# Kernel tuning notes

Measured on AMD Instinct MI355X. Metric: run time of the kernel, lower is better.

Reference implementation:

```python
import jax, jax.numpy as jnp
import numpy as np

B, S, N = 1, 128, 256
C_IN, C_H, C_OUT = 256, 32, 128
EPS = 1e-5


def setup_inputs() -> dict:
    key = jax.random.key(0)
    k_m, k_wa, k_wb, k_wo = jax.random.split(key, 4)
    m = jax.random.normal(k_m, (B, S, N, C_IN), dtype=jnp.float32)
    mask = jnp.ones((B, S, N), dtype=jnp.float32)
    gamma = jnp.ones((C_IN,), dtype=jnp.float32)
    beta = jnp.zeros((C_IN,), dtype=jnp.float32)
    # nn.Linear weights are (out, in)
    Wa = jax.random.normal(k_wa, (C_H, C_IN), dtype=jnp.float32) / np.sqrt(C_IN).astype(np.float32)
    Wb = jax.random.normal(k_wb, (C_H, C_IN), dtype=jnp.float32) / np.sqrt(C_IN).astype(np.float32)
    # proj_o is final_init (zeros) in the source; use small random weights so the
    # baseline output is non-trivial for correctness checking.
    Wo = jax.random.normal(k_wo, (C_OUT, C_H * C_H), dtype=jnp.float32) / np.sqrt(C_H * C_H).astype(np.float32)
    bo = jnp.zeros((C_OUT,), dtype=jnp.float32)
    return {"m": m, "mask": mask, "gamma": gamma, "beta": beta,
            "Wa": Wa, "Wb": Wb, "Wo": Wo, "bo": bo}


def reference(m, mask, gamma, beta, Wa, Wb, Wo, bo):
    # LayerNorm over c_in
    mu = jnp.mean(m, axis=-1, keepdims=True)
    var = jnp.mean((m - mu) ** 2, axis=-1, keepdims=True)
    mn = (m - mu) * jax.lax.rsqrt(var + EPS) * gamma + beta  # (B,S,N,c_in)

    mk = mask[..., None]  # (B,S,N,1)
    a = jnp.einsum('bsni,hi->bsnh', mn, Wa) * mk  # (B,S,N,c_h)
    b = jnp.einsum('bsni,hi->bsnh', mn, Wb) * mk  # (B,S,N,c_h)

    # pairwise mask count over S, clamped to >= 1
    num_mask = jnp.clip(jnp.einsum('bsi,bsj->bij', mask, mask), 1.0, None)  # (B,N,N)

    # outer-product mean over the sequence dim
    z = jnp.einsum('bsic,bsjd->bijcd', a, b)  # (B,N,N,c_h,c_h)
    z = z.reshape(z.shape[0], z.shape[1], z.shape[2], C_H * C_H)
    z = z / num_mask[..., None]

    return jnp.einsum('bijk,ok->bijo', z, Wo) + bo  # (B,N,N,c_out)
```

## Files before the change

### kernel.cpp

```cpp
#include <hip/hip_runtime.h>
#include <hip/hip_bf16.h>

#define S_DIM 128
#define N_DIM 256
#define CIN   256
#define CH    32
#define COUT  128

typedef __attribute__((ext_vector_type(8))) short bf16x8;
typedef __attribute__((ext_vector_type(4))) float f32x4;
typedef __attribute__((ext_vector_type(16))) float f32x16;

__device__ __forceinline__ unsigned short f2bf(float f) {
  union { float f; unsigned int u; } v; v.f = f;
  unsigned int u = v.u;
  return (unsigned short)((u + 0x7FFFu + ((u >> 16) & 1u)) >> 16);
}

__device__ __forceinline__ unsigned int pk2(float x, float y) {
  float2 f2; f2.x = x; f2.y = y;
  __hip_bfloat162 h = __float22bfloat162_rn(f2);
  union { __hip_bfloat162 h; unsigned int u; } c; c.h = h;
  return c.u;
}

__global__ __launch_bounds__(256) void lnp_prep_kernel(
    const float* __restrict__ m, const float* __restrict__ mask,
    const float* __restrict__ gamma, const float* __restrict__ beta,
    const float* __restrict__ Wa, const float* __restrict__ Wb,
    const float* __restrict__ Wo,
    float* __restrict__ rnm, unsigned short* __restrict__ wo3,
    unsigned short* __restrict__ a_t, unsigned short* __restrict__ b_t) {
  const int b = blockIdx.x, t = threadIdx.x;
  if (b < 1024) {
    __shared__ __align__(16) unsigned short mn[32][264];
    __shared__ __align__(16) unsigned short wabs[64 * 256];
    const int i = b & 255, s0 = (b >> 8) * 32;
    const int w = t >> 6, l = t & 63, lq = l >> 4, lr = l & 15;

    #pragma unroll
    for (int it = 0; it < 8; it++) {
      const int gi = it * 256 + t;
      const int r = gi >> 5, g = gi & 31;
      const float* src = (r < 32) ? (Wa + r * 256 + g * 8)
                                  : (Wb + (r - 32) * 256 + g * 8);
      const int gp = (g & 16) | ((g ^ (r & 15)) & 15);
      unsigned short* dst = &wabs[r * 256 + gp * 8];
      const float4 v0 = *(const float4*)(src);
      const float4 v1 = *(const float4*)(src + 4);
      dst[0] = f2bf(v0.x); dst[1] = f2bf(v0.y); dst[2] = f2bf(v0.z); dst[3] = f2bf(v0.w);
      dst[4] = f2bf(v1.x); dst[5] = f2bf(v1.y); dst[6] = f2bf(v1.z); dst[7] = f2bf(v1.w);
    }

    const float4 g4 = *(const float4*)(gamma + l * 4);
    const float4 b4 = *(const float4*)(beta + l * 4);

    for (int rr = 0; rr < 8; rr++) {
      const int r = w * 8 + rr;
      const int s = s0 + r;
      const float4 v = *(const float4*)(m + ((size_t)(s * N_DIM + i)) * CIN + l * 4);
      float sum = v.x + v.y + v.z + v.w;
      float sq  = v.x * v.x + v.y * v.y + v.z * v.z + v.w * v.w;
      #pragma unroll
      for (int off = 32; off > 0; off >>= 1) {
        sum += __shfl_down(sum, off);
        sq  += __shfl_down(sq, off);
      }
      sum = __shfl(sum, 0); sq = __shfl(sq, 0);
      const float mu = sum * (1.0f / CIN);
      const float var = fmaxf(sq * (1.0f / CIN) - mu * mu, 0.0f);
      const float rs = rsqrtf(var + 1e-5f);
      const float mk = mask[s * N_DIM + i];
      ushort4 p;
      p.x = f2bf(((v.x - mu) * rs * g4.x + b4.x) * mk);
      p.y = f2bf(((v.y - mu) * rs * g4.y + b4.y) * mk);
      p.z = f2bf(((v.z - mu) * rs * g4.z + b4.z) * mk);
      p.w = f2bf(((v.w - mu) * rs * g4.w + b4.w) * mk);
      *(ushort4*)(&mn[r][l * 4]) = p;
    }
    __syncthreads();

    const int wm = w & 1;
    const int n2 = w >> 1;
    f32x4 acc0 = {0.f, 0.f, 0.f, 0.f}, acc1 = {0.f, 0.f, 0.f, 0.f};
    #pragma unroll
    for (int ks = 0; ks < 8; ks++) {
      const int k0 = ks * 32 + lq * 8;
      const int g = ks * 4 + lq;
      const int gp = (g & 16) | ((g ^ lr) & 15);
      const bf16x8 af = *(const bf16x8*)(&mn[wm * 16 + lr][k0]);
      const bf16x8 bf0 = *(const bf16x8*)(&wabs[(n2 * 32 + lr) * 256 + gp * 8]);
      const bf16x8 bf1 = *(const bf16x8*)(&wabs[(n2 * 32 + 16 + lr) * 256 + gp * 8]);
      acc0 = __builtin_amdgcn_mfma_f32_16x16x32_bf16(af, bf0, acc0, 0, 0, 0);
      acc1 = __builtin_amdgcn_mfma_f32_16x16x32_bf16(af, bf1, acc1, 0, 0, 0);
    }

    unsigned short* dst = (n2 == 0) ? a_t : b_t;
    const int scol = s0 + wm * 16 + lq * 4;
    ushort4 q0, q1;
    q0.x = f2bf(acc0[0]); q0.y = f2bf(acc0[1]); q0.z = f2bf(acc0[2]); q0.w = f2bf(acc0[3]);
    q1.x = f2bf(acc1[0]); q1.y = f2bf(acc1[1]); q1.z = f2bf(acc1[2]); q1.w = f2bf(acc1[3]);
    *(ushort4*)(dst + ((size_t)(i * CH + lr)) * S_DIM + scol) = q0;
    *(ushort4*)(dst + ((size_t)(i * CH + 16 + lr)) * S_DIM + scol) = q1;
  } else if (b < 1152) {
    const int r = b - 1024;
    #pragma unroll
    for (int q = 0; q < 4; q++) {
      const int f = r * 1024 + q * 256 + t;
      const int e = f & 7, l = (f >> 3) & 63;
      const int step = (f >> 9) & 63, og = f >> 15;
      const int kp = step * 16 + (l >> 5) * 8 + e;
      const int c = kp & 31, d = kp >> 5;
      const int o = og * 32 + (l & 31);
      wo3[f] = f2bf(Wo[o * 1024 + c * 32 + d]);
    }
  } else {
    const int i = b - 1152;
    float acc = 0.f;
    #pragma unroll 8
    for (int s = 0; s < S_DIM; s++)
      acc += mask[s * N_DIM + i] * mask[s * N_DIM + t];
    acc = fmaxf(acc, 1.0f);
    rnm[i * N_DIM + t] = 1.0f / acc;
  }
}

__global__ __launch_bounds__(512, 4) void fused_kernel(
    const unsigned short* __restrict__ a_t, const unsigned short* __restrict__ b_t,
    const unsigned short* __restrict__ wo3, const float* __restrict__ rnm,
    const float* __restrict__ bo, float* __restrict__ out) {
  extern __shared__ __align__(16) unsigned short smem[];
  unsigned short* sA = smem;
  unsigned short* sB = smem + 16384;
  unsigned short* sZ = smem;
  float* fpart = (float*)smem;

  const int t = threadIdx.x, w = t >> 6, l = t & 63;
  const int lq = l >> 4, lr = l & 15;
  const int bx = blockIdx.x, by = blockIdx.y;

  const unsigned short* srcA = a_t + (size_t)bx * 32768;
  const unsigned short* srcB = b_t + (size_t)by * 16384;

  const int og = w & 3, kh = w >> 2;
  const int pA = l & 31;
  const unsigned short* wop =
      wo3 + ((size_t)(og * 64 + kh * 32) * 64 + l) * 8;

  const int wy = (w >> 1) * 64, wx = (w & 1) * 64;
  f32x4 acc[4][4];
  #pragma unroll
  for (int a = 0; a < 4; a++)
    #pragma unroll
    for (int c = 0; c < 4; c++) acc[a][c] = (f32x4){0.f, 0.f, 0.f, 0.f};

  #pragma unroll 1
  for (int h = 0; h < 2; h++) {
    if (h) __syncthreads();
    #pragma unroll
    for (int it = 0; it < 4; it++) {
      const int idx = it * 512 + t;
      const int r = idx >> 3, g = idx & 7;
      const bf16x8 v = *(const bf16x8*)(srcA + r * 128 + h * 64 + g * 8);
      *(bf16x8*)(&sA[r * 64 + ((g ^ (r & 7)) << 3)]) = v;
    }
    #pragma unroll
    for (int it = 0; it < 2; it++) {
      const int idx = it * 512 + t;
      const int r = idx >> 3, g = idx & 7;
      const bf16x8 v = *(const bf16x8*)(srcB + r * 128 + h * 64 + g * 8);
      *(bf16x8*)(&sB[r * 64 + ((g ^ (r & 7)) << 3)]) = v;
    }
    __syncthreads();

    #pragma unroll
    for (int ks2 = 0; ks2 < 2; ks2++) {
      const int gi = ks2 * 4 + lq;
      bf16x8 afr[4], bfr[4];
      #pragma unroll
      for (int a = 0; a < 4; a++) {
        const int ra = wy + a * 16 + lr;
        afr[a] = *(const bf16x8*)(&sA[ra * 64 + ((gi ^ (ra & 7)) << 3)]);
        const int rb = wx + a * 16 + lr;
        bfr[a] = *(const bf16x8*)(&sB[rb * 64 + ((gi ^ (rb & 7)) << 3)]);
      }
      #pragma unroll
      for (int a = 0; a < 4; a++)
        #pragma unroll
        for (int c = 0; c < 4; c++)
          acc[a][c] = __builtin_amdgcn_mfma_f32_16x16x32_bf16(afr[a], bfr[c], acc[a][c], 0, 0, 0);
    }
  }

  bf16x8 wfb0[4], wfb1[4];
  #pragma unroll
  for (int q = 0; q < 4; q++)
    wfb0[q] = *(const bf16x8*)(wop + (size_t)q * 512);

  __syncthreads();

  #pragma unroll
  for (int a = 0; a < 4; a++) {
    #pragma unroll
    for (int c = 0; c < 4; c++) {
      const int zrb = wy + a * 16 + lq * 4;
      const int zc  = wx + c * 16 + lr;
      const int pr = (zrb >> 5) * 4 + (zc >> 5);
      const int off = (zc & 31) * 32 + (zrb & 31);
      const int g = off >> 3;
      const int gp = (g & ~7) | ((g ^ (g >> 3) ^ pr) & 7);
      uint2 q;
      q.x = pk2(acc[a][c][0], acc[a][c][1]);
      q.y = pk2(acc[a][c][2], acc[a][c][3]);
      *(uint2*)(&sZ[pr * 1024 + gp * 8 + (off & 7)]) = q;
    }
  }
  __syncthreads();

  #pragma unroll
  for (int q = 0; q < 4; q++)
    wfb1[q] = *(const bf16x8*)(wop + (size_t)(4 + q) * 512);

  const int pair = t >> 4;
  const int ob   = (t & 15) * 8;
  const int ii = bx * 8 + (pair >> 2), jj = by * 4 + (pair & 3);
  const float sc = rnm[ii * N_DIM + jj];
  const float4 bo0 = *(const float4*)(bo + ob);
  const float4 bo1 = *(const float4*)(bo + ob + 4);

  f32x16 acc2;
  #pragma unroll
  for (int r = 0; r < 16; r++) acc2[r] = 0.f;

  #pragma unroll
  for (int jb = 0; jb < 8; jb++) {
    #pragma unroll
    for (int q = 0; q < 4; q++) {
      const int j = jb * 4 + q;
      const int s = kh * 32 + j;
      const int g = s * 2 + (l >> 5);
      const int gA = (g & ~7) | ((g ^ (g >> 3) ^ pA) & 7);
      const bf16x8 zf = *(const bf16x8*)(&sZ[pA * 1024 + gA * 8]);
      const bf16x8 wf = (jb & 1) ? wfb1[q] : wfb0[q];
      acc2 = __builtin_amdgcn_mfma_f32_32x32x16_bf16(zf, wf, acc2, 0, 0, 0);
    }
    if (jb < 6) {
      #pragma unroll
      for (int q = 0; q < 4; q++) {
        const bf16x8 v = *(const bf16x8*)(wop + (size_t)((jb + 2) * 4 + q) * 512);
        if (jb & 1) wfb1[q] = v; else wfb0[q] = v;
      }
    }
  }
  __syncthreads();

  const int oc = og * 32 + (l & 31);
  #pragma unroll
  for (int r = 0; r < 16; r++) {
    const int row = (r & 3) + 8 * (r >> 2) + 4 * (l >> 5);
    fpart[kh * 4224 + row * 132 + oc] = acc2[r];
  }
  __syncthreads();

  const int fb = pair * 132 + ob;
  f32x4 u0 = {0.f, 0.f, 0.f, 0.f}, u1 = {0.f, 0.f, 0.f, 0.f};
  #pragma unroll
  for (int q = 0; q < 2; q++) {
    u0 += *(const f32x4*)(&fpart[q * 4224 + fb]);
    u1 += *(const f32x4*)(&fpart[q * 4224 + fb + 4]);
  }
  float* po = out + ((size_t)(ii * N_DIM + jj)) * COUT + ob;
  float4 w0, w1;
  w0.x = u0[0] * sc + bo0.x; w0.y = u0[1] * sc + bo0.y;
  w0.z = u0[2] * sc + bo0.z; w0.w = u0[3] * sc + bo0.w;
  w1.x = u1[0] * sc + bo1.x; w1.y = u1[1] * sc + bo1.y;
  w1.z = u1[2] * sc + bo1.z; w1.w = u1[3] * sc + bo1.w;
  *(float4*)(po)     = w0;
  *(float4*)(po + 4) = w1;
}

extern "C" void kernel_launch(void* const* d_in, const int* in_sizes, int n_in,
                              void* d_out, int out_size, void* d_ws, size_t ws_size,
                              hipStream_t stream) {
  const float* m     = (const float*)d_in[0];
  const float* mask  = (const float*)d_in[1];
  const float* gamma = (const float*)d_in[2];
  const float* beta  = (const float*)d_in[3];
  const float* Wa    = (const float*)d_in[4];
  const float* Wb    = (const float*)d_in[5];
  const float* Wo    = (const float*)d_in[6];
  const float* bo    = (const float*)d_in[7];
  float* out = (float*)d_out;

  char* ws = (char*)d_ws;
  float*          rnm = (float*)(ws);
  unsigned short* wo3 = (unsigned short*)(ws + 262144);
  unsigned short* a_t = (unsigned short*)(ws + 524288);
  unsigned short* b_t = (unsigned short*)(ws + 2621440);

  hipFuncSetAttribute((const void*)fused_kernel,
                      hipFuncAttributeMaxDynamicSharedMemorySize, 65536);

  lnp_prep_kernel<<<1408, 256, 0, stream>>>(m, mask, gamma, beta, Wa, Wb, Wo,
                                            rnm, wo3, a_t, b_t);
  fused_kernel<<<dim3(32, 64), 512, 65536, stream>>>(a_t, b_t, wo3, rnm, bo, out);
}
```

Measured before the change: 144.6 us.

## Double-buffer S-chunk loads in fused kernel and pack bf16 conversions in prep

The fused outer-product kernel now splits the S=128 reduction into four 32-wide chunks held in two ping-pong LDS buffers. The global loads for the next chunk are issued into registers before the MFMA work on the current chunk, so load latency overlaps compute instead of stalling between halves. The prep kernel now converts to bf16 with paired conversions written as vector stores, and issues all eight row loads of m and mask before the LayerNorm math. The cost is one more barrier per chunk, more live registers, and more complex LDS indexing.

```diff
diff --git a/kernel.cpp b/kernel.cpp
--- a/kernel.cpp
+++ b/kernel.cpp
@@ -45,20 +45,30 @@
       const float* src = (r < 32) ? (Wa + r * 256 + g * 8)
                                   : (Wb + (r - 32) * 256 + g * 8);
       const int gp = (g & 16) | ((g ^ (r & 15)) & 15);
-      unsigned short* dst = &wabs[r * 256 + gp * 8];
       const float4 v0 = *(const float4*)(src);
       const float4 v1 = *(const float4*)(src + 4);
-      dst[0] = f2bf(v0.x); dst[1] = f2bf(v0.y); dst[2] = f2bf(v0.z); dst[3] = f2bf(v0.w);
-      dst[4] = f2bf(v1.x); dst[5] = f2bf(v1.y); dst[6] = f2bf(v1.z); dst[7] = f2bf(v1.w);
+      uint4 qv;
+      qv.x = pk2(v0.x, v0.y); qv.y = pk2(v0.z, v0.w);
+      qv.z = pk2(v1.x, v1.y); qv.w = pk2(v1.z, v1.w);
+      *(uint4*)(&wabs[r * 256 + gp * 8]) = qv;
     }
 
     const float4 g4 = *(const float4*)(gamma + l * 4);
     const float4 b4 = *(const float4*)(beta + l * 4);
 
+    float4 mv[8];
+    float mkv[8];
+    #pragma unroll
+    for (int rr = 0; rr < 8; rr++) {
+      const int s = s0 + w * 8 + rr;
+      mv[rr] = *(const float4*)(m + ((size_t)(s * N_DIM + i)) * CIN + l * 4);
+      mkv[rr] = mask[s * N_DIM + i];
+    }
+
+    #pragma unroll
     for (int rr = 0; rr < 8; rr++) {
       const int r = w * 8 + rr;
-      const int s = s0 + r;
-      const float4 v = *(const float4*)(m + ((size_t)(s * N_DIM + i)) * CIN + l * 4);
+      const float4 v = mv[rr];
       float sum = v.x + v.y + v.z + v.w;
       float sq  = v.x * v.x + v.y * v.y + v.z * v.z + v.w * v.w;
       #pragma unroll
@@ -70,13 +80,13 @@
       const float mu = sum * (1.0f / CIN);
       const float var = fmaxf(sq * (1.0f / CIN) - mu * mu, 0.0f);
       const float rs = rsqrtf(var + 1e-5f);
-      const float mk = mask[s * N_DIM + i];
-      ushort4 p;
-      p.x = f2bf(((v.x - mu) * rs * g4.x + b4.x) * mk);
-      p.y = f2bf(((v.y - mu) * rs * g4.y + b4.y) * mk);
-      p.z = f2bf(((v.z - mu) * rs * g4.z + b4.z) * mk);
-      p.w = f2bf(((v.w - mu) * rs * g4.w + b4.w) * mk);
-      *(ushort4*)(&mn[r][l * 4]) = p;
+      const float mk = mkv[rr];
+      uint2 p2;
+      p2.x = pk2(((v.x - mu) * rs * g4.x + b4.x) * mk,
+                 ((v.y - mu) * rs * g4.y + b4.y) * mk);
+      p2.y = pk2(((v.z - mu) * rs * g4.z + b4.z) * mk,
+                 ((v.w - mu) * rs * g4.w + b4.w) * mk);
+      *(uint2*)(&mn[r][l * 4]) = p2;
     }
     __syncthreads();
 
@@ -97,11 +107,11 @@
 
     unsigned short* dst = (n2 == 0) ? a_t : b_t;
     const int scol = s0 + wm * 16 + lq * 4;
-    ushort4 q0, q1;
-    q0.x = f2bf(acc0[0]); q0.y = f2bf(acc0[1]); q0.z = f2bf(acc0[2]); q0.w = f2bf(acc0[3]);
-    q1.x = f2bf(acc1[0]); q1.y = f2bf(acc1[1]); q1.z = f2bf(acc1[2]); q1.w = f2bf(acc1[3]);
-    *(ushort4*)(dst + ((size_t)(i * CH + lr)) * S_DIM + scol) = q0;
-    *(ushort4*)(dst + ((size_t)(i * CH + 16 + lr)) * S_DIM + scol) = q1;
+    uint2 q0, q1;
+    q0.x = pk2(acc0[0], acc0[1]); q0.y = pk2(acc0[2], acc0[3]);
+    q1.x = pk2(acc1[0], acc1[1]); q1.y = pk2(acc1[2], acc1[3]);
+    *(uint2*)(dst + ((size_t)(i * CH + lr)) * S_DIM + scol) = q0;
+    *(uint2*)(dst + ((size_t)(i * CH + 16 + lr)) * S_DIM + scol) = q1;
   } else if (b < 1152) {
     const int r = b - 1024;
     #pragma unroll
@@ -130,8 +140,10 @@
     const unsigned short* __restrict__ wo3, const float* __restrict__ rnm,
     const float* __restrict__ bo, float* __restrict__ out) {
   extern __shared__ __align__(16) unsigned short smem[];
-  unsigned short* sA = smem;
-  unsigned short* sB = smem + 16384;
+  unsigned short* sA0 = smem;
+  unsigned short* sA1 = smem + 8192;
+  unsigned short* sB0 = smem + 16384;
+  unsigned short* sB1 = smem + 20480;
   unsigned short* sZ = smem;
   float* fpart = (float*)smem;
 
@@ -154,50 +166,62 @@
     #pragma unroll
     for (int c = 0; c < 4; c++) acc[a][c] = (f32x4){0.f, 0.f, 0.f, 0.f};
 
-  #pragma unroll 1
-  for (int h = 0; h < 2; h++) {
-    if (h) __syncthreads();
-    #pragma unroll
-    for (int it = 0; it < 4; it++) {
-      const int idx = it * 512 + t;
-      const int r = idx >> 3, g = idx & 7;
-      const bf16x8 v = *(const bf16x8*)(srcA + r * 128 + h * 64 + g * 8);
-      *(bf16x8*)(&sA[r * 64 + ((g ^ (r & 7)) << 3)]) = v;
-    }
-    #pragma unroll
-    for (int it = 0; it < 2; it++) {
-      const int idx = it * 512 + t;
-      const int r = idx >> 3, g = idx & 7;
-      const bf16x8 v = *(const bf16x8*)(srcB + r * 128 + h * 64 + g * 8);
-      *(bf16x8*)(&sB[r * 64 + ((g ^ (r & 7)) << 3)]) = v;
-    }
-    __syncthreads();
-
-    #pragma unroll
-    for (int ks2 = 0; ks2 < 2; ks2++) {
-      const int gi = ks2 * 4 + lq;
-      bf16x8 afr[4], bfr[4];
-      #pragma unroll
-      for (int a = 0; a < 4; a++) {
-        const int ra = wy + a * 16 + lr;
-        afr[a] = *(const bf16x8*)(&sA[ra * 64 + ((gi ^ (ra & 7)) << 3)]);
-        const int rb = wx + a * 16 + lr;
-        bfr[a] = *(const bf16x8*)(&sB[rb * 64 + ((gi ^ (rb & 7)) << 3)]);
-      }
-      #pragma unroll
-      for (int a = 0; a < 4; a++)
-        #pragma unroll
-        for (int c = 0; c < 4; c++)
-          acc[a][c] = __builtin_amdgcn_mfma_f32_16x16x32_bf16(afr[a], bfr[c], acc[a][c], 0, 0, 0);
-    }
-  }
+  bf16x8 ldA0, ldA1, ldB0;
+  const int sr = t >> 2, sg = t & 3;
+  const int swz = ((sg ^ sr) & 3) << 3;
+
+#define ISSUE_CH(c) do { \
+    ldA0 = *(const bf16x8*)(srcA + sr * 128 + (c) * 32 + sg * 8); \
+    ldA1 = *(const bf16x8*)(srcA + (128 + sr) * 128 + (c) * 32 + sg * 8); \
+    ldB0 = *(const bf16x8*)(srcB + sr * 128 + (c) * 32 + sg * 8); \
+  } while (0)
+
+#define WRITE_CH(c) do { \
+    unsigned short* dA = ((c) & 1) ? sA1 : sA0; \
+    unsigned short* dB = ((c) & 1) ? sB1 : sB0; \
+    *(bf16x8*)(&dA[sr * 32 + swz]) = ldA0; \
+    *(bf16x8*)(&dA[(128 + sr) * 32 + swz]) = ldA1; \
+    *(bf16x8*)(&dB[sr * 32 + swz]) = ldB0; \
+  } while (0)
+
+#define COMPUTE_CH(c) do { \
+    const unsigned short* pa = ((c) & 1) ? sA1 : sA0; \
+    const unsigned short* pb = ((c) & 1) ? sB1 : sB0; \
+    bf16x8 afr[4], bfr[4]; \
+    _Pragma("unroll") \
+    for (int a2 = 0; a2 < 4; a2++) { \
+      const int ra = wy + a2 * 16 + lr; \
+      afr[a2] = *(const bf16x8*)(&pa[ra * 32 + (((lq ^ ra) & 3) << 3)]); \
+      const int rb = wx + a2 * 16 + lr; \
+      bfr[a2] = *(const bf16x8*)(&pb[rb * 32 + (((lq ^ rb) & 3) << 3)]); \
+    } \
+    _Pragma("unroll") \
+    for (int a2 = 0; a2 < 4; a2++) \
+      _Pragma("unroll") \
+      for (int c2 = 0; c2 < 4; c2++) \
+        acc[a2][c2] = __builtin_amdgcn_mfma_f32_16x16x32_bf16(afr[a2], bfr[c2], acc[a2][c2], 0, 0, 0); \
+  } while (0)
+
+  ISSUE_CH(0);
+  WRITE_CH(0);
+  ISSUE_CH(1);
+  __syncthreads();
+
+  WRITE_CH(1); ISSUE_CH(2); COMPUTE_CH(0); __syncthreads();
+  WRITE_CH(2); ISSUE_CH(3); COMPUTE_CH(1); __syncthreads();
+  WRITE_CH(3);              COMPUTE_CH(2); __syncthreads();
 
   bf16x8 wfb0[4], wfb1[4];
   #pragma unroll
   for (int q = 0; q < 4; q++)
     wfb0[q] = *(const bf16x8*)(wop + (size_t)q * 512);
 
-  __syncthreads();
+  COMPUTE_CH(3);
+  __syncthreads();
+
+#undef ISSUE_CH
+#undef WRITE_CH
+#undef COMPUTE_CH
 
   #pragma unroll
   for (int a = 0; a < 4; a++) {
```

Result: slower. 154.8 us (+7.0%).

## Drop split-K reduction in output projection; vectorize bf16 packing and batch loads

Applied to the files above, without the earlier changes.

The second GEMM stage (z times Wo) now runs on only 4 waves, each covering the full K=1024 instead of half, which removes the LDS partial-sum buffer, two barriers and the cross-wave reduction. Each wave writes its outputs directly to global memory with per-element scale and bias, so stores become scalar and strided rather than float4. The prep kernel packs bf16 pairs with wide LDS/global stores and issues all LayerNorm row loads up front to raise memory-level parallelism. The trade-off is that half the waves sit idle in the second GEMM and the dependent MFMA chain doubles in length.

```diff
diff --git a/kernel.cpp b/kernel.cpp
--- a/kernel.cpp
+++ b/kernel.cpp
@@ -45,20 +45,30 @@
       const float* src = (r < 32) ? (Wa + r * 256 + g * 8)
                                   : (Wb + (r - 32) * 256 + g * 8);
       const int gp = (g & 16) | ((g ^ (r & 15)) & 15);
-      unsigned short* dst = &wabs[r * 256 + gp * 8];
       const float4 v0 = *(const float4*)(src);
       const float4 v1 = *(const float4*)(src + 4);
-      dst[0] = f2bf(v0.x); dst[1] = f2bf(v0.y); dst[2] = f2bf(v0.z); dst[3] = f2bf(v0.w);
-      dst[4] = f2bf(v1.x); dst[5] = f2bf(v1.y); dst[6] = f2bf(v1.z); dst[7] = f2bf(v1.w);
+      uint4 qv;
+      qv.x = pk2(v0.x, v0.y); qv.y = pk2(v0.z, v0.w);
+      qv.z = pk2(v1.x, v1.y); qv.w = pk2(v1.z, v1.w);
+      *(uint4*)(&wabs[r * 256 + gp * 8]) = qv;
     }
 
     const float4 g4 = *(const float4*)(gamma + l * 4);
     const float4 b4 = *(const float4*)(beta + l * 4);
 
+    float4 mv[8];
+    float mkv[8];
+    #pragma unroll
+    for (int rr = 0; rr < 8; rr++) {
+      const int s = s0 + w * 8 + rr;
+      mv[rr] = *(const float4*)(m + ((size_t)(s * N_DIM + i)) * CIN + l * 4);
+      mkv[rr] = mask[s * N_DIM + i];
+    }
+
+    #pragma unroll
     for (int rr = 0; rr < 8; rr++) {
       const int r = w * 8 + rr;
-      const int s = s0 + r;
-      const float4 v = *(const float4*)(m + ((size_t)(s * N_DIM + i)) * CIN + l * 4);
+      const float4 v = mv[rr];
       float sum = v.x + v.y + v.z + v.w;
       float sq  = v.x * v.x + v.y * v.y + v.z * v.z + v.w * v.w;
       #pragma unroll
@@ -70,13 +80,13 @@
       const float mu = sum * (1.0f / CIN);
       const float var = fmaxf(sq * (1.0f / CIN) - mu * mu, 0.0f);
       const float rs = rsqrtf(var + 1e-5f);
-      const float mk = mask[s * N_DIM + i];
-      ushort4 p;
-      p.x = f2bf(((v.x - mu) * rs * g4.x + b4.x) * mk);
-      p.y = f2bf(((v.y - mu) * rs * g4.y + b4.y) * mk);
-      p.z = f2bf(((v.z - mu) * rs * g4.z + b4.z) * mk);
-      p.w = f2bf(((v.w - mu) * rs * g4.w + b4.w) * mk);
-      *(ushort4*)(&mn[r][l * 4]) = p;
+      const float mk = mkv[rr];
+      uint2 p2;
+      p2.x = pk2(((v.x - mu) * rs * g4.x + b4.x) * mk,
+                 ((v.y - mu) * rs * g4.y + b4.y) * mk);
+      p2.y = pk2(((v.z - mu) * rs * g4.z + b4.z) * mk,
+                 ((v.w - mu) * rs * g4.w + b4.w) * mk);
+      *(uint2*)(&mn[r][l * 4]) = p2;
     }
     __syncthreads();
 
@@ -97,11 +107,11 @@
 
     unsigned short* dst = (n2 == 0) ? a_t : b_t;
     const int scol = s0 + wm * 16 + lq * 4;
-    ushort4 q0, q1;
-    q0.x = f2bf(acc0[0]); q0.y = f2bf(acc0[1]); q0.z = f2bf(acc0[2]); q0.w = f2bf(acc0[3]);
-    q1.x = f2bf(acc1[0]); q1.y = f2bf(acc1[1]); q1.z = f2bf(acc1[2]); q1.w = f2bf(acc1[3]);
-    *(ushort4*)(dst + ((size_t)(i * CH + lr)) * S_DIM + scol) = q0;
-    *(ushort4*)(dst + ((size_t)(i * CH + 16 + lr)) * S_DIM + scol) = q1;
+    uint2 q0, q1;
+    q0.x = pk2(acc0[0], acc0[1]); q0.y = pk2(acc0[2], acc0[3]);
+    q1.x = pk2(acc1[0], acc1[1]); q1.y = pk2(acc1[2], acc1[3]);
+    *(uint2*)(dst + ((size_t)(i * CH + lr)) * S_DIM + scol) = q0;
+    *(uint2*)(dst + ((size_t)(i * CH + 16 + lr)) * S_DIM + scol) = q1;
   } else if (b < 1152) {
     const int r = b - 1024;
     #pragma unroll
@@ -133,7 +143,6 @@
   unsigned short* sA = smem;
   unsigned short* sB = smem + 16384;
   unsigned short* sZ = smem;
-  float* fpart = (float*)smem;
 
   const int t = threadIdx.x, w = t >> 6, l = t & 63;
   const int lq = l >> 4, lr = l & 15;
@@ -142,10 +151,9 @@
   const unsigned short* srcA = a_t + (size_t)bx * 32768;
   const unsigned short* srcB = b_t + (size_t)by * 16384;
 
-  const int og = w & 3, kh = w >> 2;
+  const int og = w & 3;
   const int pA = l & 31;
-  const unsigned short* wop =
-      wo3 + ((size_t)(og * 64 + kh * 32) * 64 + l) * 8;
+  const unsigned short* wop = wo3 + ((size_t)(og * 64) * 64 + l) * 8;
 
   const int wy = (w >> 1) * 64, wx = (w & 1) * 64;
   f32x4 acc[4][4];
@@ -193,9 +201,11 @@
   }
 
   bf16x8 wfb0[4], wfb1[4];
-  #pragma unroll
-  for (int q = 0; q < 4; q++)
-    wfb0[q] = *(const bf16x8*)(wop + (size_t)q * 512);
+  if (w < 4) {
+    #pragma unroll
+    for (int q = 0; q < 4; q++)
+      wfb0[q] = *(const bf16x8*)(wop + (size_t)q * 512);
+  }
 
   __syncthreads();
 
@@ -217,34 +227,38 @@
   }
   __syncthreads();
 
+  if (w >= 4) return;
+
   #pragma unroll
   for (int q = 0; q < 4; q++)
     wfb1[q] = *(const bf16x8*)(wop + (size_t)(4 + q) * 512);
 
-  const int pair = t >> 4;
-  const int ob   = (t & 15) * 8;
-  const int ii = bx * 8 + (pair >> 2), jj = by * 4 + (pair & 3);
-  const float sc = rnm[ii * N_DIM + jj];
-  const float4 bo0 = *(const float4*)(bo + ob);
-  const float4 bo1 = *(const float4*)(bo + ob + 4);
+  const int o = og * 32 + (l & 31);
+  const float bov = bo[o];
+  float scv[16];
+  #pragma unroll
+  for (int r = 0; r < 16; r++) {
+    const int row = (r & 3) + 8 * (r >> 2) + 4 * (l >> 5);
+    const int ii = bx * 8 + (row >> 2), jj = by * 4 + (row & 3);
+    scv[r] = rnm[ii * N_DIM + jj];
+  }
 
   f32x16 acc2;
   #pragma unroll
   for (int r = 0; r < 16; r++) acc2[r] = 0.f;
 
   #pragma unroll
-  for (int jb = 0; jb < 8; jb++) {
+  for (int jb = 0; jb < 16; jb++) {
     #pragma unroll
     for (int q = 0; q < 4; q++) {
-      const int j = jb * 4 + q;
-      const int s = kh * 32 + j;
+      const int s = jb * 4 + q;
       const int g = s * 2 + (l >> 5);
       const int gA = (g & ~7) | ((g ^ (g >> 3) ^ pA) & 7);
       const bf16x8 zf = *(const bf16x8*)(&sZ[pA * 1024 + gA * 8]);
       const bf16x8 wf = (jb & 1) ? wfb1[q] : wfb0[q];
       acc2 = __builtin_amdgcn_mfma_f32_32x32x16_bf16(zf, wf, acc2, 0, 0, 0);
     }
-    if (jb < 6) {
+    if (jb < 14) {
       #pragma unroll
       for (int q = 0; q < 4; q++) {
         const bf16x8 v = *(const bf16x8*)(wop + (size_t)((jb + 2) * 4 + q) * 512);
@@ -252,31 +266,13 @@
       }
     }
   }
-  __syncthreads();
-
-  const int oc = og * 32 + (l & 31);
+
   #pragma unroll
   for (int r = 0; r < 16; r++) {
     const int row = (r & 3) + 8 * (r >> 2) + 4 * (l >> 5);
-    fpart[kh * 4224 + row * 132 + oc] = acc2[r];
-  }
-  __syncthreads();
-
-  const int fb = pair * 132 + ob;
-  f32x4 u0 = {0.f, 0.f, 0.f, 0.f}, u1 = {0.f, 0.f, 0.f, 0.f};
-  #pragma unroll
-  for (int q = 0; q < 2; q++) {
-    u0 += *(const f32x4*)(&fpart[q * 4224 + fb]);
-    u1 += *(const f32x4*)(&fpart[q * 4224 + fb + 4]);
-  }
-  float* po = out + ((size_t)(ii * N_DIM + jj)) * COUT + ob;
-  float4 w0, w1;
-  w0.x = u0[0] * sc + bo0.x; w0.y = u0[1] * sc + bo0.y;
-  w0.z = u0[2] * sc + bo0.z; w0.w = u0[3] * sc + bo0.w;
-  w1.x = u1[0] * sc + bo1.x; w1.y = u1[1] * sc + bo1.y;
-  w1.z = u1[2] * sc + bo1.z; w1.w = u1[3] * sc + bo1.w;
-  *(float4*)(po)     = w0;
-  *(float4*)(po + 4) = w1;
+    const int ii = bx * 8 + (row >> 2), jj = by * 4 + (row & 3);
+    out[((size_t)(ii * N_DIM + jj)) * COUT + o] = acc2[r] * scv[r] + bov;
+  }
 }
 
 extern "C" void kernel_launch(void* const* d_in, const int* in_sizes, int n_in,
```

Result: faster. 139.9 us (median of 2 runs) (-3.3%).
